# Kernel tuning notes

Measured on AMD Instinct MI355X. Metric: run time of the kernel, lower is better.

Reference implementation:

```python
import jax, jax.numpy as jnp
import numpy as np

B, S, D, H = 1, 2048, 768, 12
WIN = 128            # window_size
HALF = WIN // 2      # 64
WN = WIN + 1         # each position attends to [i-64, i+64] inclusive -> 129 keys
DH = D // H


def setup_inputs() -> dict:
    key = jax.random.key(0)
    ks = jax.random.split(key, 8)
    scale = 0.02
    return {
        "query": jax.random.normal(ks[0], (B, S, D), dtype=jnp.float32),
        "key":   jax.random.normal(ks[1], (B, S, D), dtype=jnp.float32),
        "value": jax.random.normal(ks[2], (B, S, D), dtype=jnp.float32),
        "Wq": jax.random.normal(ks[3], (D, D), dtype=jnp.float32) * scale,
        "bq": jnp.zeros((D,), dtype=jnp.float32),
        "Wk": jax.random.normal(ks[4], (D, D), dtype=jnp.float32) * scale,
        "bk": jnp.zeros((D,), dtype=jnp.float32),
        "Wv": jax.random.normal(ks[5], (D, D), dtype=jnp.float32) * scale,
        "bv": jnp.zeros((D,), dtype=jnp.float32),
        "Wo": jax.random.normal(ks[6], (D, D), dtype=jnp.float32) * scale,
        "bo": jnp.zeros((D,), dtype=jnp.float32),
    }


def reference(query, key, value, Wq, bq, Wk, bk, Wv, bv, Wo, bo):
    b, s, d = query.shape
    # Linear projections, split heads: [B,S,H,DH]
    q = (query @ Wq + bq).reshape(b, s, H, DH)
    k = (key   @ Wk + bk).reshape(b, s, H, DH)
    v = (value @ Wv + bv).reshape(b, s, H, DH)

    # Window gather indices: pos[i, j] = i - HALF + j, j in [0, WN)
    pos = jnp.arange(s)[:, None] + (jnp.arange(WN)[None, :] - HALF)  # [S, WN]
    valid = (pos >= 0) & (pos < s)                                   # [S, WN]
    idx = jnp.clip(pos, 0, s - 1)

    kw = k[:, idx]  # [B, S, WN, H, DH]
    vw = v[:, idx]  # [B, S, WN, H, DH]

    scores = jnp.einsum('bshd,bswhd->bhsw', q, kw) / np.sqrt(DH)     # [B,H,S,WN]
    scores = jnp.where(valid[None, None, :, :], scores, -jnp.inf)
    attn = jax.nn.softmax(scores, axis=-1)

    ctx = jnp.einsum('bhsw,bswhd->bshd', attn, vw).reshape(b, s, d)  # [B,S,D]
    return ctx @ Wo + bo
```

## Files before the change

kernel.cpp:

```cpp
#include <hip/hip_runtime.h>
#include <math.h>

#define S_LEN 2048
#define DM 768
#define NHEAD 12
#define DHEAD 64
#define HALF_W 64

typedef _Float16 half8 __attribute__((ext_vector_type(8)));
typedef _Float16 half4_t __attribute__((ext_vector_type(4)));
typedef float floatx4 __attribute__((ext_vector_type(4)));

typedef const __attribute__((address_space(1))) unsigned int* gas_ptr;
typedef __attribute__((address_space(3))) unsigned int* las_ptr;
__device__ __forceinline__ void gld_lds16(const void* g, void* l) {
  __builtin_amdgcn_global_load_lds((gas_ptr)g, (las_ptr)l, 16, 0, 0);
}

__global__ __launch_bounds__(256)
void prep_w_kernel(const float* __restrict__ Wq, const float* __restrict__ Wk,
                   const float* __restrict__ Wv, const float* __restrict__ Wo,
                   _Float16* __restrict__ Tq, _Float16* __restrict__ Tk,
                   _Float16* __restrict__ Tv, _Float16* __restrict__ To) {
  __shared__ float t[64][65];
  int b = blockIdx.x;
  int z = b / 144, rem = b % 144;
  const float* W = z == 0 ? Wq : z == 1 ? Wk : z == 2 ? Wv : Wo;
  _Float16* T = z == 0 ? Tq : z == 1 ? Tk : z == 2 ? Tv : To;
  int n0 = (rem % 12) * 64, k0 = (rem / 12) * 64;
  int tx = threadIdx.x & 15, ty = threadIdx.x >> 4;
#pragma unroll
  for (int i = 0; i < 4; ++i) {
    int row = ty + i * 16;
    float4 v = *(const float4*)(W + (size_t)(k0 + row) * DM + n0 + tx * 4);
    t[row][tx * 4 + 0] = v.x; t[row][tx * 4 + 1] = v.y;
    t[row][tx * 4 + 2] = v.z; t[row][tx * 4 + 3] = v.w;
  }
  __syncthreads();
#pragma unroll
  for (int i = 0; i < 4; ++i) {
    int nn = ty + i * 16, kk = tx * 4;
    half4_t h = {(_Float16)t[kk + 0][nn], (_Float16)t[kk + 1][nn],
                 (_Float16)t[kk + 2][nn], (_Float16)t[kk + 3][nn]};
    *(half4_t*)(T + (size_t)(n0 + nn) * DM + k0 + kk) = h;
  }
}

#define GBM 64
#define GBN 64
#define GBK 64

__global__ __launch_bounds__(256, 4)
void gemm_qkv_kernel(const float* __restrict__ A0, const float* __restrict__ A1,
                     const float* __restrict__ A2, const _Float16* __restrict__ W0,
                     const _Float16* __restrict__ W1, const _Float16* __restrict__ W2,
                     const float* __restrict__ b0, const float* __restrict__ b1,
                     const float* __restrict__ b2, _Float16* __restrict__ Q,
                     _Float16* __restrict__ K, _Float16* __restrict__ Vt) {
  __shared__ __align__(16) _Float16 As[GBM * GBK];
  __shared__ __align__(16) _Float16 Bs[GBN * GBK];
  const int z = blockIdx.z;
  const float* A = z == 0 ? A0 : z == 1 ? A1 : A2;
  const _Float16* Wt = z == 0 ? W0 : z == 1 ? W1 : W2;
  const float* bias = z == 0 ? b0 : z == 1 ? b1 : b2;

  const int tid = threadIdx.x;
  const int lane = tid & 63;
  const int w = tid >> 6;
  const int lr = lane & 15;
  const int lq = lane >> 4;
  const int wm = w >> 1, wn = w & 1;
  const int m0 = blockIdx.y * GBM;
  const int n0 = blockIdx.x * GBN;
  const int wb = tid & 192;

  floatx4 acc[2][2] = {};

  for (int k0 = 0; k0 < DM; k0 += GBK) {
    __syncthreads();
#pragma unroll
    for (int i = 0; i < 2; ++i) {
      int c = i * 256 + tid;
      int m = c >> 3, j = c & 7;
      const float* src = A + (size_t)(m0 + m) * DM + k0 + j * 8;
      float4 v0 = *(const float4*)src;
      float4 v1 = *(const float4*)(src + 4);
      half8 h = {(_Float16)v0.x, (_Float16)v0.y, (_Float16)v0.z, (_Float16)v0.w,
                 (_Float16)v1.x, (_Float16)v1.y, (_Float16)v1.z, (_Float16)v1.w};
      *(half8*)&As[(m * 8 + (j ^ (m & 7))) * 8] = h;
    }
#pragma unroll
    for (int i = 0; i < 2; ++i) {
      int c = i * 256 + tid;
      int n = c >> 3, j = c & 7, jg = j ^ (n & 7);
      gld_lds16(Wt + (size_t)(n0 + n) * DM + k0 + jg * 8, &Bs[(i * 256 + wb) * 8]);
    }
    __syncthreads();

#pragma unroll
    for (int kh = 0; kh < 2; ++kh) {
      half8 af[2], bf[2];
#pragma unroll
      for (int mt = 0; mt < 2; ++mt) {
        int m = wm * 32 + mt * 16 + lr;
        int j = (kh * 4 + lq) ^ (m & 7);
        af[mt] = *(const half8*)&As[m * GBK + j * 8];
      }
#pragma unroll
      for (int nt = 0; nt < 2; ++nt) {
        int n = wn * 32 + nt * 16 + lr;
        int j = (kh * 4 + lq) ^ (n & 7);
        bf[nt] = *(const half8*)&Bs[n * GBK + j * 8];
      }
#pragma unroll
      for (int mt = 0; mt < 2; ++mt)
#pragma unroll
        for (int nt = 0; nt < 2; ++nt)
          acc[mt][nt] = __builtin_amdgcn_mfma_f32_16x16x32_f16(af[mt], bf[nt], acc[mt][nt], 0, 0, 0);
    }
  }

#pragma unroll
  for (int mt = 0; mt < 2; ++mt) {
    int row0 = m0 + wm * 32 + mt * 16 + lq * 4;
#pragma unroll
    for (int nt = 0; nt < 2; ++nt) {
      int col = n0 + wn * 32 + nt * 16 + lr;
      float bv = bias[col];
      if (z == 2) {
        half4_t o = {(_Float16)(acc[mt][nt][0] + bv), (_Float16)(acc[mt][nt][1] + bv),
                     (_Float16)(acc[mt][nt][2] + bv), (_Float16)(acc[mt][nt][3] + bv)};
        *(half4_t*)(Vt + (size_t)col * S_LEN + row0) = o;
      } else {
        _Float16* H = z == 0 ? Q : K;
#pragma unroll
        for (int rr = 0; rr < 4; ++rr)
          H[(size_t)(row0 + rr) * DM + col] = (_Float16)(acc[mt][nt][rr] + bv);
      }
    }
  }
}

__global__ __launch_bounds__(256, 4)
void gemm_out_kernel(const _Float16* __restrict__ A, const _Float16* __restrict__ Wt,
                     const float* __restrict__ bias, float* __restrict__ C) {
  __shared__ __align__(16) _Float16 As[GBM * GBK];
  __shared__ __align__(16) _Float16 Bs[GBN * GBK];
  const int tid = threadIdx.x;
  const int lane = tid & 63;
  const int w = tid >> 6;
  const int lr = lane & 15;
  const int lq = lane >> 4;
  const int wm = w >> 1, wn = w & 1;
  const int m0 = blockIdx.y * GBM;
  const int n0 = blockIdx.x * GBN;
  const int wb = tid & 192;

  floatx4 acc[2][2] = {};

  for (int k0 = 0; k0 < DM; k0 += GBK) {
    __syncthreads();
#pragma unroll
    for (int i = 0; i < 2; ++i) {
      int c = i * 256 + tid;
      int m = c >> 3, j = c & 7, jg = j ^ (m & 7);
      gld_lds16(A + (size_t)(m0 + m) * DM + k0 + jg * 8, &As[(i * 256 + wb) * 8]);
    }
#pragma unroll
    for (int i = 0; i < 2; ++i) {
      int c = i * 256 + tid;
      int n = c >> 3, j = c & 7, jg = j ^ (n & 7);
      gld_lds16(Wt + (size_t)(n0 + n) * DM + k0 + jg * 8, &Bs[(i * 256 + wb) * 8]);
    }
    __syncthreads();

#pragma unroll
    for (int kh = 0; kh < 2; ++kh) {
      half8 af[2], bf[2];
#pragma unroll
      for (int mt = 0; mt < 2; ++mt) {
        int m = wm * 32 + mt * 16 + lr;
        int j = (kh * 4 + lq) ^ (m & 7);
        af[mt] = *(const half8*)&As[m * GBK + j * 8];
      }
#pragma unroll
      for (int nt = 0; nt < 2; ++nt) {
        int n = wn * 32 + nt * 16 + lr;
        int j = (kh * 4 + lq) ^ (n & 7);
        bf[nt] = *(const half8*)&Bs[n * GBK + j * 8];
      }
#pragma unroll
      for (int mt = 0; mt < 2; ++mt)
#pragma unroll
        for (int nt = 0; nt < 2; ++nt)
          acc[mt][nt] = __builtin_amdgcn_mfma_f32_16x16x32_f16(af[mt], bf[nt], acc[mt][nt], 0, 0, 0);
    }
  }

#pragma unroll
  for (int mt = 0; mt < 2; ++mt) {
    int row0 = m0 + wm * 32 + mt * 16 + lq * 4;
#pragma unroll
    for (int nt = 0; nt < 2; ++nt) {
      int col = n0 + wn * 32 + nt * 16 + lr;
      float bv = bias[col];
#pragma unroll
      for (int rr = 0; rr < 4; ++rr)
        C[(size_t)(row0 + rr) * DM + col] = acc[mt][nt][rr] + bv;
    }
  }
}

#define ATQ 32
#define AR 160
#define VTC 24

__global__ __launch_bounds__(256, 2)
void swattn_mfma_kernel(const _Float16* __restrict__ qh, const _Float16* __restrict__ kh,
                        const _Float16* __restrict__ vt, _Float16* __restrict__ ctx) {
  __shared__ __align__(16) _Float16 Qs[ATQ * DHEAD];
  __shared__ __align__(16) _Float16 Ks[AR * DHEAD];
  __shared__ __align__(16) _Float16 Vs[DHEAD * VTC * 8];
  __shared__ float Sbuf[ATQ][161];
  __shared__ __align__(16) _Float16 Pbuf[ATQ][168];

  const int tid = threadIdx.x;
  const int lane = tid & 63, w = tid >> 6;
  const int lr = lane & 15, lq = lane >> 4;
  const int s0 = blockIdx.x * ATQ;
  const int h = blockIdx.y;
  const int wb = tid & 192;

  {
    int r = tid >> 3, j = tid & 7;
    int jg = j ^ (r & 7);
    gld_lds16(qh + (size_t)(s0 + r) * DM + h * DHEAD + jg * 8, &Qs[wb * 8]);
  }
#pragma unroll
  for (int i = 0; i < 5; ++i) {
    int c = i * 256 + tid;
    int r = c >> 3, j = c & 7;
    int jg = j ^ (r & 7);
    int pos = s0 - HALF_W + r;
    pos = pos < 0 ? 0 : (pos > S_LEN - 1 ? S_LEN - 1 : pos);
    gld_lds16(kh + (size_t)pos * DM + h * DHEAD + jg * 8, &Ks[(i * 256 + wb) * 8]);
  }
#pragma unroll
  for (int i = 0; i < 6; ++i) {
    int c = i * 256 + tid;
    if (c < 1536) {
      int r = c / VTC, j = c % VTC;
      int jg = j ^ (r & 7);
      int cb = s0 - HALF_W + jg * 8;
      cb = cb < 0 ? 0 : (cb > S_LEN - 8 ? S_LEN - 8 : cb);
      gld_lds16(vt + (size_t)(h * DHEAD + r) * S_LEN + cb, &Vs[(i * 256 + wb) * 8]);
    }
  }
  __syncthreads();

  {
    const int qt = w >> 1;
    const int ptb = (w & 1) * 5;
    half8 aq[2];
#pragma unroll
    for (int k2 = 0; k2 < 2; ++k2) {
      int r = qt * 16 + lr, j = (k2 * 4 + lq) ^ (r & 7);
      aq[k2] = *(const half8*)&Qs[r * DHEAD + j * 8];
    }
#pragma unroll
    for (int i = 0; i < 5; ++i) {
      int pt = ptb + i;
      floatx4 acc = {};
#pragma unroll
      for (int k2 = 0; k2 < 2; ++k2) {
        int r = pt * 16 + lr, j = (k2 * 4 + lq) ^ (r & 7);
        half8 bk2 = *(const half8*)&Ks[r * DHEAD + j * 8];
        acc = __builtin_amdgcn_mfma_f32_16x16x32_f16(aq[k2], bk2, acc, 0, 0, 0);
      }
#pragma unroll
      for (int rr = 0; rr < 4; ++rr)
        Sbuf[qt * 16 + lq * 4 + rr][pt * 16 + lr] = acc[rr] * 0.125f;
    }
  }
  __syncthreads();

#pragma unroll
  for (int i = 0; i < 8; ++i) {
    int q = w * 8 + i;
    int p0 = lane, p1 = 64 + lane, p2 = 128 + lane;
    int g0 = s0 - HALF_W + p0, g1 = s0 + lane, g2 = s0 + HALF_W + lane;
    bool ok0 = (p0 >= q) && (g0 >= 0);
    bool ok1 = (g1 < S_LEN);
    bool ok2 = (lane <= q) && (g2 < S_LEN);
    float sv0 = ok0 ? Sbuf[q][p0] : -1e30f;
    float sv1 = ok1 ? Sbuf[q][p1] : -1e30f;
    float sv2 = ok2 ? Sbuf[q][p2] : -1e30f;
    float mx = fmaxf(sv0, fmaxf(sv1, sv2));
#pragma unroll
    for (int off = 32; off > 0; off >>= 1) mx = fmaxf(mx, __shfl_xor(mx, off, 64));
    float e0 = __expf(sv0 - mx), e1 = __expf(sv1 - mx), e2 = __expf(sv2 - mx);
    float sum = e0 + e1 + e2;
#pragma unroll
    for (int off = 32; off > 0; off >>= 1) sum += __shfl_xor(sum, off, 64);
    float inv = 1.f / sum;
    Pbuf[q][p0] = (_Float16)(e0 * inv);
    Pbuf[q][p1] = (_Float16)(e1 * inv);
    if (lane < 32) Pbuf[q][p2] = (_Float16)(e2 * inv);
  }
  __syncthreads();

  {
    const int qt = w >> 1;
    const int dt0 = (w & 1) * 2;
    floatx4 a0 = {}, a1 = {};
#pragma unroll
    for (int ks = 0; ks < 5; ++ks) {
      half8 ap = *(const half8*)&Pbuf[qt * 16 + lr][ks * 32 + lq * 8];
      int r0 = dt0 * 16 + lr, r1 = (dt0 + 1) * 16 + lr;
      int j0 = (ks * 4 + lq) ^ (r0 & 7), j1 = (ks * 4 + lq) ^ (r1 & 7);
      half8 bv0 = *(const half8*)&Vs[(r0 * VTC + j0) * 8];
      half8 bv1 = *(const half8*)&Vs[(r1 * VTC + j1) * 8];
      a0 = __builtin_amdgcn_mfma_f32_16x16x32_f16(ap, bv0, a0, 0, 0, 0);
      a1 = __builtin_amdgcn_mfma_f32_16x16x32_f16(ap, bv1, a1, 0, 0, 0);
    }
#pragma unroll
    for (int rr = 0; rr < 4; ++rr) {
      size_t row = (size_t)(s0 + qt * 16 + lq * 4 + rr) * DM + h * DHEAD;
      ctx[row + dt0 * 16 + lr] = (_Float16)a0[rr];
      ctx[row + (dt0 + 1) * 16 + lr] = (_Float16)a1[rr];
    }
  }
}

extern "C" void kernel_launch(void* const* d_in, const int* in_sizes, int n_in,
                              void* d_out, int out_size, void* d_ws, size_t ws_size,
                              hipStream_t stream) {
  const float* query = (const float*)d_in[0];
  const float* key   = (const float*)d_in[1];
  const float* value = (const float*)d_in[2];
  const float* Wq = (const float*)d_in[3];
  const float* bq = (const float*)d_in[4];
  const float* Wk = (const float*)d_in[5];
  const float* bk = (const float*)d_in[6];
  const float* Wv = (const float*)d_in[7];
  const float* bv = (const float*)d_in[8];
  const float* Wo = (const float*)d_in[9];
  const float* bo = (const float*)d_in[10];
  float* out = (float*)d_out;

  const size_t nel = (size_t)S_LEN * DM;
  const size_t wel = (size_t)DM * DM;
  _Float16* Wtq = (_Float16*)d_ws;
  _Float16* Wtk = Wtq + wel;
  _Float16* Wtv = Wtk + wel;
  _Float16* Wto = Wtv + wel;
  _Float16* qh = Wto + wel;
  _Float16* khb = qh + nel;
  _Float16* Vtg = khb + nel;
  _Float16* ctxh = Vtg + nel;

  prep_w_kernel<<<dim3(576), 256, 0, stream>>>(Wq, Wk, Wv, Wo, Wtq, Wtk, Wtv, Wto);
  gemm_qkv_kernel<<<dim3(DM / GBN, S_LEN / GBM, 3), 256, 0, stream>>>(
      query, key, value, Wtq, Wtk, Wtv, bq, bk, bv, qh, khb, Vtg);
  swattn_mfma_kernel<<<dim3(S_LEN / ATQ, NHEAD), 256, 0, stream>>>(qh, khb, Vtg, ctxh);
  gemm_out_kernel<<<dim3(DM / GBN, S_LEN / GBM), 256, 0, stream>>>(ctxh, Wto, bo, out);
}
```

Before: 142.6 us.

## Keep attention scores in registers, async-load fp32 A tiles, raise occupancy bounds

The attention kernel now keeps QK^T scores in MFMA accumulator registers and does the softmax with shuffles plus a small cross-wave reduction buffer. This removes the fp32 score buffer in LDS, reuses the Q buffer for probabilities, and uses a padded unswizzled V layout. Blocks are launched on a 1D grid remapped so that neighbouring blocks cover interleaved sequence tiles. The QKV GEMM now loads fp32 activations straight into LDS with async global_load_lds and converts them to fp16 when reading fragments, which doubles the A tile's LDS footprint. Launch-bounds occupancy hints are raised for all three kernels, which may force register spilling.

```diff
diff --git a/kernel.cpp b/kernel.cpp
--- a/kernel.cpp
+++ b/kernel.cpp
@@ -50,14 +50,14 @@
 #define GBN 64
 #define GBK 64
 
-__global__ __launch_bounds__(256, 4)
+__global__ __launch_bounds__(256, 6)
 void gemm_qkv_kernel(const float* __restrict__ A0, const float* __restrict__ A1,
                      const float* __restrict__ A2, const _Float16* __restrict__ W0,
                      const _Float16* __restrict__ W1, const _Float16* __restrict__ W2,
                      const float* __restrict__ b0, const float* __restrict__ b1,
                      const float* __restrict__ b2, _Float16* __restrict__ Q,
                      _Float16* __restrict__ K, _Float16* __restrict__ Vt) {
-  __shared__ __align__(16) _Float16 As[GBM * GBK];
+  __shared__ __align__(16) float Asf[GBM * GBK];
   __shared__ __align__(16) _Float16 Bs[GBN * GBK];
   const int z = blockIdx.z;
   const float* A = z == 0 ? A0 : z == 1 ? A1 : A2;
@@ -79,15 +79,10 @@
   for (int k0 = 0; k0 < DM; k0 += GBK) {
     __syncthreads();
 #pragma unroll
-    for (int i = 0; i < 2; ++i) {
+    for (int i = 0; i < 4; ++i) {
       int c = i * 256 + tid;
-      int m = c >> 3, j = c & 7;
-      const float* src = A + (size_t)(m0 + m) * DM + k0 + j * 8;
-      float4 v0 = *(const float4*)src;
-      float4 v1 = *(const float4*)(src + 4);
-      half8 h = {(_Float16)v0.x, (_Float16)v0.y, (_Float16)v0.z, (_Float16)v0.w,
-                 (_Float16)v1.x, (_Float16)v1.y, (_Float16)v1.z, (_Float16)v1.w};
-      *(half8*)&As[(m * 8 + (j ^ (m & 7))) * 8] = h;
+      int m = c >> 4, j = c & 15, jg = j ^ (m & 14);
+      gld_lds16(A + (size_t)(m0 + m) * DM + k0 + jg * 4, &Asf[(i * 256 + wb) * 4]);
     }
 #pragma unroll
     for (int i = 0; i < 2; ++i) {
@@ -103,8 +98,11 @@
 #pragma unroll
       for (int mt = 0; mt < 2; ++mt) {
         int m = wm * 32 + mt * 16 + lr;
-        int j = (kh * 4 + lq) ^ (m & 7);
-        af[mt] = *(const half8*)&As[m * GBK + j * 8];
+        int j0 = (kh * 8 + lq * 2) ^ (m & 14);
+        float4 f0 = *(const float4*)&Asf[(m * 16 + j0) * 4];
+        float4 f1 = *(const float4*)&Asf[(m * 16 + j0 + 1) * 4];
+        af[mt] = half8{(_Float16)f0.x, (_Float16)f0.y, (_Float16)f0.z, (_Float16)f0.w,
+                       (_Float16)f1.x, (_Float16)f1.y, (_Float16)f1.z, (_Float16)f1.w};
       }
 #pragma unroll
       for (int nt = 0; nt < 2; ++nt) {
@@ -141,7 +139,7 @@
   }
 }
 
-__global__ __launch_bounds__(256, 4)
+__global__ __launch_bounds__(256, 6)
 void gemm_out_kernel(const _Float16* __restrict__ A, const _Float16* __restrict__ Wt,
                      const float* __restrict__ bias, float* __restrict__ C) {
   __shared__ __align__(16) _Float16 As[GBM * GBK];
@@ -212,35 +210,31 @@
 }
 
 #define ATQ 32
-#define AR 160
-#define VTC 24
-
-__global__ __launch_bounds__(256, 2)
+
+__global__ __launch_bounds__(256, 3)
 void swattn_mfma_kernel(const _Float16* __restrict__ qh, const _Float16* __restrict__ kh,
                         const _Float16* __restrict__ vt, _Float16* __restrict__ ctx) {
-  __shared__ __align__(16) _Float16 Qs[ATQ * DHEAD];
-  __shared__ __align__(16) _Float16 Ks[AR * DHEAD];
-  __shared__ __align__(16) _Float16 Vs[DHEAD * VTC * 8];
-  __shared__ float Sbuf[ATQ][161];
-  __shared__ __align__(16) _Float16 Pbuf[ATQ][168];
+  __shared__ __align__(16) _Float16 Ks[160 * 64];
+  __shared__ __align__(16) _Float16 Vs[64 * 168];
+  __shared__ __align__(16) _Float16 QP[32 * 168];
+  __shared__ float red[4][32];
 
   const int tid = threadIdx.x;
   const int lane = tid & 63, w = tid >> 6;
   const int lr = lane & 15, lq = lane >> 4;
-  const int s0 = blockIdx.x * ATQ;
-  const int h = blockIdx.y;
+  const int bid = blockIdx.x;
+  const int x = bid & 7, mid = (bid >> 3) & 7, h = bid >> 6;
+  const int s0 = (x * 8 + mid) * ATQ;
   const int wb = tid & 192;
 
   {
-    int r = tid >> 3, j = tid & 7;
-    int jg = j ^ (r & 7);
-    gld_lds16(qh + (size_t)(s0 + r) * DM + h * DHEAD + jg * 8, &Qs[wb * 8]);
+    int r = tid >> 3, j = tid & 7, jg = j ^ (r & 7);
+    gld_lds16(qh + (size_t)(s0 + r) * DM + h * DHEAD + jg * 8, &QP[wb * 8]);
   }
 #pragma unroll
   for (int i = 0; i < 5; ++i) {
     int c = i * 256 + tid;
-    int r = c >> 3, j = c & 7;
-    int jg = j ^ (r & 7);
+    int r = c >> 3, j = c & 7, jg = j ^ (r & 7);
     int pos = s0 - HALF_W + r;
     pos = pos < 0 ? 0 : (pos > S_LEN - 1 ? S_LEN - 1 : pos);
     gld_lds16(kh + (size_t)pos * DM + h * DHEAD + jg * 8, &Ks[(i * 256 + wb) * 8]);
@@ -248,84 +242,110 @@
 #pragma unroll
   for (int i = 0; i < 6; ++i) {
     int c = i * 256 + tid;
-    if (c < 1536) {
-      int r = c / VTC, j = c % VTC;
-      int jg = j ^ (r & 7);
-      int cb = s0 - HALF_W + jg * 8;
+    if (c < 1344) {
+      int r = c / 21, j = c % 21;
+      int cb = s0 - HALF_W + j * 8;
       cb = cb < 0 ? 0 : (cb > S_LEN - 8 ? S_LEN - 8 : cb);
       gld_lds16(vt + (size_t)(h * DHEAD + r) * S_LEN + cb, &Vs[(i * 256 + wb) * 8]);
     }
   }
   __syncthreads();
 
+  const int qt = w & 1, ph = w >> 1;
+  floatx4 sc[5];
   {
-    const int qt = w >> 1;
-    const int ptb = (w & 1) * 5;
     half8 aq[2];
 #pragma unroll
     for (int k2 = 0; k2 < 2; ++k2) {
       int r = qt * 16 + lr, j = (k2 * 4 + lq) ^ (r & 7);
-      aq[k2] = *(const half8*)&Qs[r * DHEAD + j * 8];
-    }
-#pragma unroll
-    for (int i = 0; i < 5; ++i) {
-      int pt = ptb + i;
-      floatx4 acc = {};
+      aq[k2] = *(const half8*)&QP[r * DHEAD + j * 8];
+    }
+#pragma unroll
+    for (int t = 0; t < 5; ++t) {
+      int pt = ph * 5 + t;
+      floatx4 a = {};
 #pragma unroll
       for (int k2 = 0; k2 < 2; ++k2) {
         int r = pt * 16 + lr, j = (k2 * 4 + lq) ^ (r & 7);
-        half8 bk2 = *(const half8*)&Ks[r * DHEAD + j * 8];
-        acc = __builtin_amdgcn_mfma_f32_16x16x32_f16(aq[k2], bk2, acc, 0, 0, 0);
-      }
-#pragma unroll
-      for (int rr = 0; rr < 4; ++rr)
-        Sbuf[qt * 16 + lq * 4 + rr][pt * 16 + lr] = acc[rr] * 0.125f;
-    }
-  }
-  __syncthreads();
-
-#pragma unroll
-  for (int i = 0; i < 8; ++i) {
-    int q = w * 8 + i;
-    int p0 = lane, p1 = 64 + lane, p2 = 128 + lane;
-    int g0 = s0 - HALF_W + p0, g1 = s0 + lane, g2 = s0 + HALF_W + lane;
-    bool ok0 = (p0 >= q) && (g0 >= 0);
-    bool ok1 = (g1 < S_LEN);
-    bool ok2 = (lane <= q) && (g2 < S_LEN);
-    float sv0 = ok0 ? Sbuf[q][p0] : -1e30f;
-    float sv1 = ok1 ? Sbuf[q][p1] : -1e30f;
-    float sv2 = ok2 ? Sbuf[q][p2] : -1e30f;
-    float mx = fmaxf(sv0, fmaxf(sv1, sv2));
-#pragma unroll
-    for (int off = 32; off > 0; off >>= 1) mx = fmaxf(mx, __shfl_xor(mx, off, 64));
-    float e0 = __expf(sv0 - mx), e1 = __expf(sv1 - mx), e2 = __expf(sv2 - mx);
-    float sum = e0 + e1 + e2;
-#pragma unroll
-    for (int off = 32; off > 0; off >>= 1) sum += __shfl_xor(sum, off, 64);
-    float inv = 1.f / sum;
-    Pbuf[q][p0] = (_Float16)(e0 * inv);
-    Pbuf[q][p1] = (_Float16)(e1 * inv);
-    if (lane < 32) Pbuf[q][p2] = (_Float16)(e2 * inv);
+        half8 bk = *(const half8*)&Ks[r * DHEAD + j * 8];
+        a = __builtin_amdgcn_mfma_f32_16x16x32_f16(aq[k2], bk, a, 0, 0, 0);
+      }
+      sc[t] = a;
+    }
+  }
+
+  const int qbase = qt * 16 + lq * 4;
+  float m4[4] = {-1e30f, -1e30f, -1e30f, -1e30f};
+#pragma unroll
+  for (int t = 0; t < 5; ++t) {
+    int p = (ph * 5 + t) * 16 + lr;
+    int g = s0 - HALF_W + p;
+#pragma unroll
+    for (int rr = 0; rr < 4; ++rr) {
+      int q = qbase + rr;
+      bool ok = (p >= q) && (p <= q + 128) && (g >= 0) && (g < S_LEN);
+      float v = ok ? sc[t][rr] * 0.125f : -1e30f;
+      sc[t][rr] = v;
+      m4[rr] = fmaxf(m4[rr], v);
+    }
+  }
+#pragma unroll
+  for (int off = 1; off <= 8; off <<= 1)
+#pragma unroll
+    for (int rr = 0; rr < 4; ++rr) m4[rr] = fmaxf(m4[rr], __shfl_xor(m4[rr], off, 64));
+  if (lr == 0)
+#pragma unroll
+    for (int rr = 0; rr < 4; ++rr) red[ph][qbase + rr] = m4[rr];
+  __syncthreads();
+
+  float ss[4] = {0.f, 0.f, 0.f, 0.f};
+  float mm[4];
+#pragma unroll
+  for (int rr = 0; rr < 4; ++rr)
+    mm[rr] = fmaxf(red[0][qbase + rr], red[1][qbase + rr]);
+#pragma unroll
+  for (int t = 0; t < 5; ++t)
+#pragma unroll
+    for (int rr = 0; rr < 4; ++rr) {
+      float e = __expf(sc[t][rr] - mm[rr]);
+      sc[t][rr] = e;
+      ss[rr] += e;
+    }
+#pragma unroll
+  for (int off = 1; off <= 8; off <<= 1)
+#pragma unroll
+    for (int rr = 0; rr < 4; ++rr) ss[rr] += __shfl_xor(ss[rr], off, 64);
+  if (lr == 0)
+#pragma unroll
+    for (int rr = 0; rr < 4; ++rr) red[2 + ph][qbase + rr] = ss[rr];
+  __syncthreads();
+
+#pragma unroll
+  for (int rr = 0; rr < 4; ++rr) {
+    float inv = 1.f / (red[2][qbase + rr] + red[3][qbase + rr]);
+#pragma unroll
+    for (int t = 0; t < 5; ++t) {
+      int p = (ph * 5 + t) * 16 + lr;
+      QP[(qbase + rr) * 168 + p] = (_Float16)(sc[t][rr] * inv);
+    }
   }
   __syncthreads();
 
   {
-    const int qt = w >> 1;
-    const int dt0 = (w & 1) * 2;
+    const int qt2 = w & 1;
+    const int dt0 = (w >> 1) * 2;
     floatx4 a0 = {}, a1 = {};
 #pragma unroll
     for (int ks = 0; ks < 5; ++ks) {
-      half8 ap = *(const half8*)&Pbuf[qt * 16 + lr][ks * 32 + lq * 8];
-      int r0 = dt0 * 16 + lr, r1 = (dt0 + 1) * 16 + lr;
-      int j0 = (ks * 4 + lq) ^ (r0 & 7), j1 = (ks * 4 + lq) ^ (r1 & 7);
-      half8 bv0 = *(const half8*)&Vs[(r0 * VTC + j0) * 8];
-      half8 bv1 = *(const half8*)&Vs[(r1 * VTC + j1) * 8];
+      half8 ap = *(const half8*)&QP[(qt2 * 16 + lr) * 168 + ks * 32 + lq * 8];
+      half8 bv0 = *(const half8*)&Vs[(dt0 * 16 + lr) * 168 + ks * 32 + lq * 8];
+      half8 bv1 = *(const half8*)&Vs[((dt0 + 1) * 16 + lr) * 168 + ks * 32 + lq * 8];
       a0 = __builtin_amdgcn_mfma_f32_16x16x32_f16(ap, bv0, a0, 0, 0, 0);
       a1 = __builtin_amdgcn_mfma_f32_16x16x32_f16(ap, bv1, a1, 0, 0, 0);
     }
 #pragma unroll
     for (int rr = 0; rr < 4; ++rr) {
-      size_t row = (size_t)(s0 + qt * 16 + lq * 4 + rr) * DM + h * DHEAD;
+      size_t row = (size_t)(s0 + qt2 * 16 + lq * 4 + rr) * DM + h * DHEAD;
       ctx[row + dt0 * 16 + lr] = (_Float16)a0[rr];
       ctx[row + (dt0 + 1) * 16 + lr] = (_Float16)a1[rr];
     }
@@ -362,6 +382,6 @@
   prep_w_kernel<<<dim3(576), 256, 0, stream>>>(Wq, Wk, Wv, Wo, Wtq, Wtk, Wtv, Wto);
   gemm_qkv_kernel<<<dim3(DM / GBN, S_LEN / GBM, 3), 256, 0, stream>>>(
       query, key, value, Wtq, Wtk, Wtv, bq, bk, bv, qh, khb, Vtg);
-  swattn_mfma_kernel<<<dim3(S_LEN / ATQ, NHEAD), 256, 0, stream>>>(qh, khb, Vtg, ctxh);
+  swattn_mfma_kernel<<<dim3((S_LEN / ATQ) * NHEAD), 256, 0, stream>>>(qh, khb, Vtg, ctxh);
   gemm_out_kernel<<<dim3(DM / GBN, S_LEN / GBM), 256, 0, stream>>>(ctxh, Wto, bo, out);
 }
```

New measurement: 149.9 us. +5.1%, slower.
